# Performance work log

Measured on AMD Instinct MI355X. Metric: run time of the kernel, lower is better.

## Reference

```python
import jax, jax.numpy as jnp
import numpy as np

LOW_T = 0.05
HIGH_T = 0.15

SOBEL_X = jnp.array([[-1., 0., 1.], [-2., 0., 2.], [-1., 0., 1.]], dtype=jnp.float32).reshape(1, 1, 3, 3)
SOBEL_Y = jnp.array([[1., 2., 1.], [0., 0., 0.], [-1., -2., -1.]], dtype=jnp.float32).reshape(1, 1, 3, 3)


def _conv3x3(x, k):
    # NCHW conv, padding=1, stride=1 (matches F.conv2d(x, k, padding=1))
    return jax.lax.conv_general_dilated(x, k, window_strides=(1, 1), padding=((1, 1), (1, 1)))


def setup_inputs() -> dict:
    key = jax.random.key(0)
    x = jax.random.normal(key, (1, 1, 4096, 4096), dtype=jnp.float32)
    return {"x": x}


def reference(x):
    grad_x = _conv3x3(x, SOBEL_X)
    grad_y = _conv3x3(x, SOBEL_Y)
    grad_mag = jnp.sqrt(grad_x * grad_x + grad_y * grad_y)
    grad_dir = jnp.arctan2(grad_y, grad_x)  # radians, as in the original (compared to degree thresholds)

    m = grad_mag[0, 0]  # [H, W]
    d = grad_dir[0, 0][1:-1, 1:-1]  # direction at interior pixels [H-2, W-2]
    H, W = m.shape

    def sh(dr, dc):
        # magnitude at (row+dr, col+dc) for interior pixels
        return m[1 + dr:H - 1 + dr, 1 + dc:W - 1 + dc]

    mc = sh(0, 0)

    # Branch predicates replicated literally from the torch code (degree thresholds
    # vs radian values; some sub-conditions are vacuously false, kept for faithfulness).
    b1 = ((d >= -22.5) & (d <= 22.5)) | ((d >= 157.5) & (d <= 180.0)) | ((d >= -157.5) & (d <= -180.0))
    b2 = ((d > 22.5) & (d <= 67.5)) | ((d >= -112.5) & (d < -157.5))
    b3 = ((d > 67.5) & (d <= 112.5)) | ((d >= -67.5) & (d < -22.5))

    mag_prev = jnp.where(b1, sh(0, -1), jnp.where(b2, sh(-1, 1), jnp.where(b3, sh(-1, 0), sh(-1, -1))))
    mag_next = jnp.where(b1, sh(0, 1), jnp.where(b2, sh(1, -1), jnp.where(b3, sh(1, 0), sh(1, 1))))

    keep = (mc >= mag_prev) & (mc >= mag_next)
    interior = jnp.where(keep, mc, jnp.zeros_like(mc))
    edges = jnp.zeros_like(m).at[1:-1, 1:-1].set(interior)

    # Double thresholding: strong -> 255, weak ([low, high]) -> 0, below-low passes through.
    strong = edges > HIGH_T
    weak = (edges >= LOW_T) & (edges <= HIGH_T)
    out = jnp.where(strong, jnp.float32(255.0), jnp.where(weak, jnp.float32(0.0), edges))
    return out  # [H, W]
```

## Files before the change

kernel.cpp:

```cpp
#include <hip/hip_runtime.h>
#include <math.h>


constexpr int Wd = 4096;
constexpr int Ht = 4096;
constexpr int ROWS = 8;

typedef float f4 __attribute__((ext_vector_type(4)));
typedef float f2 __attribute__((ext_vector_type(2)));

__global__ __launch_bounds__(256) void canny_kernel(const float* __restrict__ x,
                                                    float* __restrict__ out) {
    const int tid  = threadIdx.x;
    const int lane = tid & 63;
    const int wv   = tid >> 6;
    const int wc   = blockIdx.x;
    const int cbase = wc * 256;
    const int c     = cbase + lane * 4;
    const int r0    = (blockIdx.y * 4 + wv) * ROWS;

    f4 X[ROWS + 2];
    #pragma unroll
    for (int k = 0; k < ROWS + 2; ++k) {
        int rr = r0 - 1 + k;
        rr = rr < 0 ? 0 : (rr > Ht - 1 ? Ht - 1 : rr);
        X[k] = *(const f4*)(x + (size_t)rr * Wd + c);
    }

    f2 hl = {0.f, 0.f};
    {
        const int  hk   = lane & 31;
        const bool left = lane < 32;
        const bool valid = (hk < ROWS + 2) && (left ? (wc > 0) : (wc < 15));
        if (valid) {
            int rr = r0 - 1 + hk;
            rr = rr < 0 ? 0 : (rr > Ht - 1 ? Ht - 1 : rr);
            const int hc = left ? cbase - 2 : cbase + 256;
            hl = *(const f2*)(x + (size_t)rr * Wd + hc);
        }
    }
    const float s1x = __shfl_down(hl.x, 1), s2x = __shfl_down(hl.x, 2);
    const float s1y = __shfl_down(hl.y, 1), s2y = __shfl_down(hl.y, 2);
    const float th1x = hl.x + 2.0f * s1x + s2x;
    const float th1y = hl.y + 2.0f * s1y + s2y;
    const float th2x = hl.x - s2x;
    const float th2y = hl.y - s2y;

    const float C1  = __uint_as_float(0x3CB851EDu);
    const float C2B = __uint_as_float(0x3B23D709u);

    #pragma unroll
    for (int o = 0; o < ROWS; ++o) {
        const int r = r0 + o;
        f4 a = X[o], b = X[o + 1], cc = X[o + 2];

        float t1[4], t2[4];
        #pragma unroll
        for (int j = 0; j < 4; ++j) {
            t1[j] = a[j] + 2.0f * b[j] + cc[j];
            t2[j] = a[j] - cc[j];
        }

        const int hidx = (lane == 63) ? 32 + o : o;
        const float b1x = __shfl(th1x, hidx);
        const float b1y = __shfl(th1y, hidx);
        const float b2x = __shfl(th2x, hidx);
        const float b2y = __shfl(th2y, hidx);

        float l1a = __shfl_up(t1[2], 1),   l1b = __shfl_up(t1[3], 1);
        float l2a = __shfl_up(t2[2], 1),   l2b = __shfl_up(t2[3], 1);
        float r1a = __shfl_down(t1[0], 1), r1b = __shfl_down(t1[1], 1);
        float r2a = __shfl_down(t2[0], 1), r2b = __shfl_down(t2[1], 1);
        if (lane == 0)  { l1a = b1x; l1b = b1y; l2a = b2x; l2b = b2y; }
        if (lane == 63) { r1a = b1x; r1b = b1y; r2a = b2x; r2b = b2y; }

        float T1[8] = {l1a, l1b, t1[0], t1[1], t1[2], t1[3], r1a, r1b};
        float T2[8] = {l2a, l2b, t2[0], t2[1], t2[2], t2[3], r2a, r2b};

        float q[6];
        #pragma unroll
        for (int i = 0; i < 6; ++i) {
            float gx = T1[i + 2] - T1[i];
            float gy = T2[i] + 2.0f * T2[i + 1] + T2[i + 2];
            q[i] = gx * gx + gy * gy;
        }

        bool hazard = false;
        #pragma unroll
        for (int i = 0; i < 5; ++i) {
            int d = (int)(__float_as_uint(q[i + 1]) - __float_as_uint(q[i]));
            hazard |= ((unsigned)(d + 8) < 17u);
        }

        float acc[4];
        #pragma unroll
        for (int o2 = 0; o2 < 4; ++o2) {
            float qp = q[o2], qc = q[o2 + 1], qn = q[o2 + 2];
            bool keep = (qc >= qp) && (qc >= qn);
            acc[o2] = (keep && qc > C1) ? 255.0f : 0.0f;
            hazard |= (keep && qc > 0.0f && qc <= C2B);
        }

        if (__any(hazard)) {
            float m[6];
            #pragma unroll
            for (int i = 0; i < 6; ++i) m[i] = sqrtf(q[i]);
            #pragma unroll
            for (int o2 = 0; o2 < 4; ++o2) {
                float mc = m[o2 + 1];
                bool keep = (mc >= m[o2]) && (mc >= m[o2 + 2]);
                float e = keep ? mc : 0.0f;
                acc[o2] = (e > 0.15f) ? 255.0f : ((e >= 0.05f) ? 0.0f : e);
            }
        }

        if (r == 0 || r == Ht - 1) {
            #pragma unroll
            for (int o2 = 0; o2 < 4; ++o2) acc[o2] = 0.0f;
        }
        if (wc == 0  && lane == 0)  acc[0] = 0.0f;
        if (wc == 15 && lane == 63) acc[3] = 0.0f;

        f4 v = {acc[0], acc[1], acc[2], acc[3]};
        __builtin_nontemporal_store(v, (f4*)(out + (size_t)r * Wd + c));
    }
}

extern "C" void kernel_launch(void* const* d_in, const int* in_sizes, int n_in,
                              void* d_out, int out_size, void* d_ws, size_t ws_size,
                              hipStream_t stream) {
    const float* x = (const float*)d_in[0];
    float* out = (float*)d_out;
    dim3 grid(16, 128);
    canny_kernel<<<grid, dim3(256), 0, stream>>>(x, out);
}
```

Baseline: 110.4 us.

## Process four row chunks per wave with register double-buffered prefetch

Each wave now handles 32 rows in four chunks of 8. The next chunk's rows and halo columns are loaded into registers while the current chunk is computed, and the two overlapping halo rows are carried forward so they are not reloaded. The grid shrinks fourfold. This cuts halo re-reads and hides load latency, but raises register pressure and lowers the number of waves available to hide latency.

```diff
diff --git a/kernel.cpp b/kernel.cpp
--- a/kernel.cpp
+++ b/kernel.cpp
@@ -4,7 +4,8 @@
 
 constexpr int Wd = 4096;
 constexpr int Ht = 4096;
-constexpr int ROWS = 8;
+constexpr int CH  = 8;
+constexpr int NCH = 4;
 
 typedef float f4 __attribute__((ext_vector_type(4)));
 typedef float f2 __attribute__((ext_vector_type(2)));
@@ -17,112 +18,141 @@
     const int wc   = blockIdx.x;
     const int cbase = wc * 256;
     const int c     = cbase + lane * 4;
-    const int r0    = (blockIdx.y * 4 + wv) * ROWS;
+    const int r0    = (blockIdx.y * 4 + wv) * (CH * NCH);
 
-    f4 X[ROWS + 2];
+    const int  hk     = lane & 31;
+    const bool hleft  = lane < 32;
+    const bool hvalid = (hk < CH + 2) && (hleft ? (wc > 0) : (wc < 15));
+    const int  hc     = hleft ? cbase - 2 : cbase + 256;
+
+    f4 X[CH + 2];
     #pragma unroll
-    for (int k = 0; k < ROWS + 2; ++k) {
+    for (int k = 0; k < CH + 2; ++k) {
         int rr = r0 - 1 + k;
         rr = rr < 0 ? 0 : (rr > Ht - 1 ? Ht - 1 : rr);
         X[k] = *(const f4*)(x + (size_t)rr * Wd + c);
     }
-
     f2 hl = {0.f, 0.f};
-    {
-        const int  hk   = lane & 31;
-        const bool left = lane < 32;
-        const bool valid = (hk < ROWS + 2) && (left ? (wc > 0) : (wc < 15));
-        if (valid) {
-            int rr = r0 - 1 + hk;
-            rr = rr < 0 ? 0 : (rr > Ht - 1 ? Ht - 1 : rr);
-            const int hc = left ? cbase - 2 : cbase + 256;
-            hl = *(const f2*)(x + (size_t)rr * Wd + hc);
-        }
+    if (hvalid) {
+        int rr = r0 - 1 + hk;
+        rr = rr < 0 ? 0 : rr;
+        hl = *(const f2*)(x + (size_t)rr * Wd + hc);
     }
-    const float s1x = __shfl_down(hl.x, 1), s2x = __shfl_down(hl.x, 2);
-    const float s1y = __shfl_down(hl.y, 1), s2y = __shfl_down(hl.y, 2);
-    const float th1x = hl.x + 2.0f * s1x + s2x;
-    const float th1y = hl.y + 2.0f * s1y + s2y;
-    const float th2x = hl.x - s2x;
-    const float th2y = hl.y - s2y;
 
     const float C1  = __uint_as_float(0x3CB851EDu);
     const float C2B = __uint_as_float(0x3B23D709u);
 
-    #pragma unroll
-    for (int o = 0; o < ROWS; ++o) {
-        const int r = r0 + o;
-        f4 a = X[o], b = X[o + 1], cc = X[o + 2];
+    #pragma unroll 1
+    for (int chn = 0; chn < NCH; ++chn) {
+        const int  rc   = r0 + chn * CH;
+        const bool more = (chn < NCH - 1);
 
-        float t1[4], t2[4];
-        #pragma unroll
-        for (int j = 0; j < 4; ++j) {
-            t1[j] = a[j] + 2.0f * b[j] + cc[j];
-            t2[j] = a[j] - cc[j];
-        }
-
-        const int hidx = (lane == 63) ? 32 + o : o;
-        const float b1x = __shfl(th1x, hidx);
-        const float b1y = __shfl(th1y, hidx);
-        const float b2x = __shfl(th2x, hidx);
-        const float b2y = __shfl(th2y, hidx);
-
-        float l1a = __shfl_up(t1[2], 1),   l1b = __shfl_up(t1[3], 1);
-        float l2a = __shfl_up(t2[2], 1),   l2b = __shfl_up(t2[3], 1);
-        float r1a = __shfl_down(t1[0], 1), r1b = __shfl_down(t1[1], 1);
-        float r2a = __shfl_down(t2[0], 1), r2b = __shfl_down(t2[1], 1);
-        if (lane == 0)  { l1a = b1x; l1b = b1y; l2a = b2x; l2b = b2y; }
-        if (lane == 63) { r1a = b1x; r1b = b1y; r2a = b2x; r2b = b2y; }
-
-        float T1[8] = {l1a, l1b, t1[0], t1[1], t1[2], t1[3], r1a, r1b};
-        float T2[8] = {l2a, l2b, t2[0], t2[1], t2[2], t2[3], r2a, r2b};
-
-        float q[6];
-        #pragma unroll
-        for (int i = 0; i < 6; ++i) {
-            float gx = T1[i + 2] - T1[i];
-            float gy = T2[i] + 2.0f * T2[i + 1] + T2[i + 2];
-            q[i] = gx * gx + gy * gy;
-        }
-
-        bool hazard = false;
-        #pragma unroll
-        for (int i = 0; i < 5; ++i) {
-            int d = (int)(__float_as_uint(q[i + 1]) - __float_as_uint(q[i]));
-            hazard |= ((unsigned)(d + 8) < 17u);
-        }
-
-        float acc[4];
-        #pragma unroll
-        for (int o2 = 0; o2 < 4; ++o2) {
-            float qp = q[o2], qc = q[o2 + 1], qn = q[o2 + 2];
-            bool keep = (qc >= qp) && (qc >= qn);
-            acc[o2] = (keep && qc > C1) ? 255.0f : 0.0f;
-            hazard |= (keep && qc > 0.0f && qc <= C2B);
-        }
-
-        if (__any(hazard)) {
-            float m[6];
+        f4 N[CH];
+        f2 hln = {0.f, 0.f};
+        if (more) {
             #pragma unroll
-            for (int i = 0; i < 6; ++i) m[i] = sqrtf(q[i]);
-            #pragma unroll
-            for (int o2 = 0; o2 < 4; ++o2) {
-                float mc = m[o2 + 1];
-                bool keep = (mc >= m[o2]) && (mc >= m[o2 + 2]);
-                float e = keep ? mc : 0.0f;
-                acc[o2] = (e > 0.15f) ? 255.0f : ((e >= 0.05f) ? 0.0f : e);
+            for (int k = 0; k < CH; ++k) {
+                int rr = rc + CH + 1 + k;
+                rr = rr > Ht - 1 ? Ht - 1 : rr;
+                N[k] = *(const f4*)(x + (size_t)rr * Wd + c);
+            }
+            if (hvalid) {
+                int rr = rc + CH - 1 + hk;
+                rr = rr > Ht - 1 ? Ht - 1 : rr;
+                hln = *(const f2*)(x + (size_t)rr * Wd + hc);
             }
         }
 
-        if (r == 0 || r == Ht - 1) {
+        const float s1x = __shfl_down(hl.x, 1), s2x = __shfl_down(hl.x, 2);
+        const float s1y = __shfl_down(hl.y, 1), s2y = __shfl_down(hl.y, 2);
+        const float th1x = hl.x + 2.0f * s1x + s2x;
+        const float th1y = hl.y + 2.0f * s1y + s2y;
+        const float th2x = hl.x - s2x;
+        const float th2y = hl.y - s2y;
+
+        #pragma unroll
+        for (int o = 0; o < CH; ++o) {
+            const int r = rc + o;
+            f4 a = X[o], b = X[o + 1], cc = X[o + 2];
+
+            float t1[4], t2[4];
             #pragma unroll
-            for (int o2 = 0; o2 < 4; ++o2) acc[o2] = 0.0f;
+            for (int j = 0; j < 4; ++j) {
+                t1[j] = a[j] + 2.0f * b[j] + cc[j];
+                t2[j] = a[j] - cc[j];
+            }
+
+            const int hidx = (lane == 63) ? 32 + o : o;
+            const float b1x = __shfl(th1x, hidx);
+            const float b1y = __shfl(th1y, hidx);
+            const float b2x = __shfl(th2x, hidx);
+            const float b2y = __shfl(th2y, hidx);
+
+            float l1a = __shfl_up(t1[2], 1),   l1b = __shfl_up(t1[3], 1);
+            float l2a = __shfl_up(t2[2], 1),   l2b = __shfl_up(t2[3], 1);
+            float r1a = __shfl_down(t1[0], 1), r1b = __shfl_down(t1[1], 1);
+            float r2a = __shfl_down(t2[0], 1), r2b = __shfl_down(t2[1], 1);
+            if (lane == 0)  { l1a = b1x; l1b = b1y; l2a = b2x; l2b = b2y; }
+            if (lane == 63) { r1a = b1x; r1b = b1y; r2a = b2x; r2b = b2y; }
+
+            float T1[8] = {l1a, l1b, t1[0], t1[1], t1[2], t1[3], r1a, r1b};
+            float T2[8] = {l2a, l2b, t2[0], t2[1], t2[2], t2[3], r2a, r2b};
+
+            float q[6];
+            #pragma unroll
+            for (int i = 0; i < 6; ++i) {
+                float gx = T1[i + 2] - T1[i];
+                float gy = T2[i] + 2.0f * T2[i + 1] + T2[i + 2];
+                q[i] = gx * gx + gy * gy;
+            }
+
+            bool hazard = false;
+            #pragma unroll
+            for (int i = 0; i < 5; ++i) {
+                int d = (int)(__float_as_uint(q[i + 1]) - __float_as_uint(q[i]));
+                hazard |= ((unsigned)(d + 8) < 17u);
+            }
+
+            float acc[4];
+            #pragma unroll
+            for (int o2 = 0; o2 < 4; ++o2) {
+                float qp = q[o2], qc = q[o2 + 1], qn = q[o2 + 2];
+                bool keep = (qc >= qp) && (qc >= qn);
+                acc[o2] = (keep && qc > C1) ? 255.0f : 0.0f;
+                hazard |= (keep && qc > 0.0f && qc <= C2B);
+            }
+
+            if (__any(hazard)) {
+                float m[6];
+                #pragma unroll
+                for (int i = 0; i < 6; ++i) m[i] = sqrtf(q[i]);
+                #pragma unroll
+                for (int o2 = 0; o2 < 4; ++o2) {
+                    float mc = m[o2 + 1];
+                    bool keep = (mc >= m[o2]) && (mc >= m[o2 + 2]);
+                    float e = keep ? mc : 0.0f;
+                    acc[o2] = (e > 0.15f) ? 255.0f : ((e >= 0.05f) ? 0.0f : e);
+                }
+            }
+
+            if (r == 0 || r == Ht - 1) {
+                #pragma unroll
+                for (int o2 = 0; o2 < 4; ++o2) acc[o2] = 0.0f;
+            }
+            if (wc == 0  && lane == 0)  acc[0] = 0.0f;
+            if (wc == 15 && lane == 63) acc[3] = 0.0f;
+
+            f4 v = {acc[0], acc[1], acc[2], acc[3]};
+            __builtin_nontemporal_store(v, (f4*)(out + (size_t)r * Wd + c));
         }
-        if (wc == 0  && lane == 0)  acc[0] = 0.0f;
-        if (wc == 15 && lane == 63) acc[3] = 0.0f;
 
-        f4 v = {acc[0], acc[1], acc[2], acc[3]};
-        __builtin_nontemporal_store(v, (f4*)(out + (size_t)r * Wd + c));
+        if (more) {
+            X[0] = X[CH];
+            X[1] = X[CH + 1];
+            #pragma unroll
+            for (int k = 0; k < CH; ++k) X[k + 2] = N[k];
+            hl = hln;
+        }
     }
 }
 
@@ -131,6 +161,6 @@
                               hipStream_t stream) {
     const float* x = (const float*)d_in[0];
     float* out = (float*)d_out;
-    dim3 grid(16, 128);
+    dim3 grid(16, Ht / (4 * CH * NCH));
     canny_kernel<<<grid, dim3(256), 0, stream>>>(x, out);
 }
```

Result: slower. 119.6 us (+8.3%).
